# Performance work log

Measured on AMD Instinct MI355X. Metric: run time of the kernel, lower is better.

The kernel has to match this reference:

```python
import jax, jax.numpy as jnp
import numpy as np

N_EMB = 1024
HEAD = 64
BLOCK = 2048
BATCH = 8


def setup_inputs() -> dict:
    key = jax.random.key(0)
    k_in, k_q, k_k, k_v = jax.random.split(key, 4)
    inp = jax.random.normal(k_in, (BATCH, BLOCK, N_EMB), dtype=jnp.float32)
    s = 1.0 / np.sqrt(N_EMB)
    Wq = jax.random.uniform(k_q, (N_EMB, HEAD), dtype=jnp.float32, minval=-s, maxval=s)
    Wk = jax.random.uniform(k_k, (N_EMB, HEAD), dtype=jnp.float32, minval=-s, maxval=s)
    Wv = jax.random.uniform(k_v, (N_EMB, HEAD), dtype=jnp.float32, minval=-s, maxval=s)
    return {"input": inp, "Wq": Wq, "Wk": Wk, "Wv": Wv}


def reference(input, Wq, Wk, Wv):
    # input: [B, T, E]; projections to head_size H
    q = jnp.einsum('bte,eh->bth', input, Wq)
    k = jnp.einsum('bte,eh->bth', input, Wk)
    v = jnp.einsum('bte,eh->bth', input, Wv)
    scale = 1.0 / np.sqrt(HEAD).astype(np.float32)
    # [B, T, T] causal scores
    scores = jnp.einsum('bqh,bkh->bqk', q, k) * scale
    T = input.shape[1]
    causal = jnp.tril(jnp.ones((T, T), dtype=bool))
    scores = jnp.where(causal, scores, jnp.float32(-jnp.inf))
    wei = jax.nn.softmax(scores, axis=-1)
    # dropout is identity in eval mode (p=0.1 omitted for deterministic reference)
    return jnp.einsum('bqk,bkh->bqh', wei, v)
```

## Files before the change

kernel.cpp:

```cpp
#include <hip/hip_runtime.h>
#include <hip/hip_bf16.h>
#include <math.h>

#define BATCH 8
#define SEQ   2048
#define EMB   1024
#define HEAD  64
#define BT    (BATCH * SEQ)

typedef __attribute__((ext_vector_type(8))) short  short8;
typedef __attribute__((ext_vector_type(4))) float  floatx4;

__device__ __forceinline__ unsigned short f2bf(float x) {
    union { __hip_bfloat16 h; unsigned short u; } cv;
    cv.h = __float2bfloat16(x);
    return cv.u;
}

__global__ __launch_bounds__(256) void wt_prep(
    const float* __restrict__ Wq, const float* __restrict__ Wk,
    const float* __restrict__ Wv, unsigned short* __restrict__ WT)
{
    __shared__ float tile[64][65];
    const int w  = blockIdx.x >> 4;
    const int k0 = (blockIdx.x & 15) * 64;
    const float* W = (w == 0) ? Wq : (w == 1) ? Wk : Wv;
    const int tid = threadIdx.x;

    for (int idx = tid; idx < 4096; idx += 256) {
        const int kr = idx >> 6, n = idx & 63;
        tile[kr][n] = W[(size_t)(k0 + kr) * HEAD + n];
    }
    __syncthreads();
    const int n  = tid >> 2;
    const int k8 = (tid & 3) * 16;
    unsigned short* dst = WT + (size_t)(w * 64 + n) * EMB + k0 + k8;
    short8 v0, v1;
#pragma unroll
    for (int j = 0; j < 8; ++j) v0[j] = (short)f2bf(tile[k8 + j][n]);
#pragma unroll
    for (int j = 0; j < 8; ++j) v1[j] = (short)f2bf(tile[k8 + 8 + j][n]);
    *(short8*)(dst)     = v0;
    *(short8*)(dst + 8) = v1;
}

__global__ __launch_bounds__(256) void qkv_mfma(
    const float* __restrict__ X, const unsigned short* __restrict__ WT,
    unsigned short* __restrict__ Q, unsigned short* __restrict__ K,
    unsigned short* __restrict__ VT)
{
    const int tid = threadIdx.x;
    const int l   = tid & 63;
    const int wv  = tid >> 6;
    const int g   = l >> 4,  q  = l & 15;
    const int arow = blockIdx.x * 16 + q;

    floatx4 acc[3];
#pragma unroll
    for (int nt = 0; nt < 3; ++nt) acc[nt] = (floatx4){0.f, 0.f, 0.f, 0.f};

    const float*          xp = X  + (size_t)arow * EMB + g * 8;
    const unsigned short* wp = WT + (size_t)(wv * 48 + q) * EMB + g * 8;

    float4 xa = *(const float4*)(xp);
    float4 xb = *(const float4*)(xp + 4);
    short8 w[3];
#pragma unroll
    for (int nt = 0; nt < 3; ++nt) w[nt] = *(const short8*)(wp + (size_t)nt * 16 * EMB);

    for (int k0 = 0; k0 < EMB - 32; k0 += 32) {
        float4 xa2 = *(const float4*)(xp + 32);
        float4 xb2 = *(const float4*)(xp + 36);
        short8 w2[3];
#pragma unroll
        for (int nt = 0; nt < 3; ++nt) w2[nt] = *(const short8*)(wp + 32 + (size_t)nt * 16 * EMB);
        xp += 32; wp += 32;

        short8 a;
        a[0] = (short)f2bf(xa.x); a[1] = (short)f2bf(xa.y);
        a[2] = (short)f2bf(xa.z); a[3] = (short)f2bf(xa.w);
        a[4] = (short)f2bf(xb.x); a[5] = (short)f2bf(xb.y);
        a[6] = (short)f2bf(xb.z); a[7] = (short)f2bf(xb.w);
#pragma unroll
        for (int nt = 0; nt < 3; ++nt)
            acc[nt] = __builtin_amdgcn_mfma_f32_16x16x32_bf16(a, w[nt], acc[nt], 0, 0, 0);

        xa = xa2; xb = xb2;
#pragma unroll
        for (int nt = 0; nt < 3; ++nt) w[nt] = w2[nt];
    }
    {
        short8 a;
        a[0] = (short)f2bf(xa.x); a[1] = (short)f2bf(xa.y);
        a[2] = (short)f2bf(xa.z); a[3] = (short)f2bf(xa.w);
        a[4] = (short)f2bf(xb.x); a[5] = (short)f2bf(xb.y);
        a[6] = (short)f2bf(xb.z); a[7] = (short)f2bf(xb.w);
#pragma unroll
        for (int nt = 0; nt < 3; ++nt)
            acc[nt] = __builtin_amdgcn_mfma_f32_16x16x32_bf16(a, w[nt], acc[nt], 0, 0, 0);
    }

    const int trow0 = blockIdx.x * 16 + g * 4;
#pragma unroll
    for (int nt = 0; nt < 3; ++nt) {
        const int c = wv * 48 + nt * 16 + q;
#pragma unroll
        for (int r = 0; r < 4; ++r) {
            const unsigned short v = f2bf(acc[nt][r]);
            const int t = trow0 + r;
            if (c < 64) {
                Q[(size_t)t * HEAD + c] = v;
            } else if (c < 128) {
                K[(size_t)t * HEAD + (c - 64)] = v;
            } else {
                const int bb = t >> 11, tl = t & (SEQ - 1);
                VT[((size_t)bb * HEAD + (c - 128)) * SEQ + tl] = v;
            }
        }
    }
}

__global__ __launch_bounds__(256) void attn_mfma(
    const unsigned short* __restrict__ Q, const unsigned short* __restrict__ K,
    const unsigned short* __restrict__ VT, float* __restrict__ O)
{
    __shared__ unsigned short Ks[2][64][72];
    __shared__ unsigned short Vs[2][64][72];
    __shared__ unsigned short Ps[64][72];
    __shared__ float Mo[2][16][68];
    __shared__ float Mm[2][16], Ml[2][16];

    const int tid  = threadIdx.x;
    const int l    = tid & 63;
    const int wv   = tid >> 6;
    const int pair = wv >> 1, sub = wv & 1;
    const int g    = l >> 4, q = l & 15;
    const int qt   = 63 - (blockIdx.x >> 3);
    const int b    = blockIdx.x & 7;
    const int qrow0 = qt * 32 + sub * 16;
    const size_t kbase = (size_t)b * SEQ * HEAD;
    const size_t vbase = (size_t)b * HEAD * SEQ;

    short8 bq[2];
#pragma unroll
    for (int dc = 0; dc < 2; ++dc)
        bq[dc] = *(const short8*)&Q[kbase + (size_t)(qrow0 + q) * HEAD + dc * 32 + g * 8];

    floatx4 o[4];
#pragma unroll
    for (int dt = 0; dt < 4; ++dt) o[dt] = (floatx4){0.f, 0.f, 0.f, 0.f};
    float m_run = -INFINITY, l_run = 0.f;

    const int nkt = (qt >> 1) + 1;

    short8 kreg[2], vreg[2];
#pragma unroll
    for (int i = 0; i < 2; ++i) {
        const int c = tid + i * 256, r = c >> 3, k8 = (c & 7) * 8;
        kreg[i] = *(const short8*)&K [kbase + (size_t)r * HEAD + k8];
        vreg[i] = *(const short8*)&VT[vbase + (size_t)r * SEQ  + k8];
    }

    for (int kt = 0; kt < nkt; ++kt) {
        const int bs = kt & 1;
#pragma unroll
        for (int i = 0; i < 2; ++i) {
            const int c = tid + i * 256, r = c >> 3, k8 = (c & 7) * 8;
            *(short8*)&Ks[bs][r][k8] = kreg[i];
            *(short8*)&Vs[bs][r][k8] = vreg[i];
        }
        __syncthreads();

        if (kt + 1 < nkt) {
#pragma unroll
            for (int i = 0; i < 2; ++i) {
                const int c = tid + i * 256, r = c >> 3, k8 = (c & 7) * 8;
                kreg[i] = *(const short8*)&K [kbase + (size_t)((kt + 1) * 64 + r) * HEAD + k8];
                vreg[i] = *(const short8*)&VT[vbase + (size_t)r * SEQ + (kt + 1) * 64 + k8];
            }
        }

        if ((kt & 1) == pair) {
            floatx4 s[4];
#pragma unroll
            for (int t = 0; t < 4; ++t) {
                s[t] = (floatx4){0.f, 0.f, 0.f, 0.f};
#pragma unroll
                for (int dc = 0; dc < 2; ++dc) {
                    const short8 ak = *(const short8*)&Ks[bs][t * 16 + q][dc * 32 + g * 8];
                    s[t] = __builtin_amdgcn_mfma_f32_16x16x32_bf16(ak, bq[dc], s[t], 0, 0, 0);
                }
            }

            float sv[4][4];
            if (kt == nkt - 1) {
#pragma unroll
                for (int t = 0; t < 4; ++t)
#pragma unroll
                    for (int r = 0; r < 4; ++r) {
                        const int kg = kt * 64 + t * 16 + g * 4 + r;
                        sv[t][r] = (kg > qrow0 + q) ? -INFINITY : s[t][r] * 0.125f;
                    }
            } else {
#pragma unroll
                for (int t = 0; t < 4; ++t)
#pragma unroll
                    for (int r = 0; r < 4; ++r) sv[t][r] = s[t][r] * 0.125f;
            }

            float pm = -INFINITY;
#pragma unroll
            for (int t = 0; t < 4; ++t)
#pragma unroll
                for (int r = 0; r < 4; ++r) pm = fmaxf(pm, sv[t][r]);
            pm = fmaxf(pm, __shfl_xor(pm, 16));
            pm = fmaxf(pm, __shfl_xor(pm, 32));
            const float mnew = fmaxf(m_run, pm);
            const float crow = __expf(m_run - mnew);
            float p[4][4];
            float psum = 0.f;
#pragma unroll
            for (int t = 0; t < 4; ++t)
#pragma unroll
                for (int r = 0; r < 4; ++r) {
                    p[t][r] = __expf(sv[t][r] - mnew);
                    psum += p[t][r];
                }
            psum += __shfl_xor(psum, 16);
            psum += __shfl_xor(psum, 32);
            l_run = l_run * crow + psum;
            m_run = mnew;

#pragma unroll
            for (int r = 0; r < 4; ++r) {
                const float cr = __shfl(crow, g * 4 + r);
#pragma unroll
                for (int dt = 0; dt < 4; ++dt) o[dt][r] *= cr;
            }

#pragma unroll
            for (int t = 0; t < 4; ++t) {
                const unsigned int lo = (unsigned)f2bf(p[t][0]) | ((unsigned)f2bf(p[t][1]) << 16);
                const unsigned int hi = (unsigned)f2bf(p[t][2]) | ((unsigned)f2bf(p[t][3]) << 16);
                *(unsigned int*)&Ps[wv * 16 + q][t * 16 + g * 4]     = lo;
                *(unsigned int*)&Ps[wv * 16 + q][t * 16 + g * 4 + 2] = hi;
            }
            asm volatile("s_waitcnt lgkmcnt(0)" ::: "memory");
            __builtin_amdgcn_sched_barrier(0);

#pragma unroll
            for (int kc = 0; kc < 2; ++kc) {
                const short8 pa = *(const short8*)&Ps[wv * 16 + q][kc * 32 + g * 8];
#pragma unroll
                for (int dt = 0; dt < 4; ++dt) {
                    const short8 vb = *(const short8*)&Vs[bs][dt * 16 + q][kc * 32 + g * 8];
                    o[dt] = __builtin_amdgcn_mfma_f32_16x16x32_bf16(pa, vb, o[dt], 0, 0, 0);
                }
            }
        }
    }

    __syncthreads();
    if (pair == 1) {
#pragma unroll
        for (int dt = 0; dt < 4; ++dt)
#pragma unroll
            for (int r = 0; r < 4; ++r)
                Mo[sub][g * 4 + r][dt * 16 + q] = o[dt][r];
        if (g == 0) { Mm[sub][q] = m_run; Ml[sub][q] = l_run; }
    }
    __syncthreads();
    if (pair == 0) {
        const float m1  = Mm[sub][q];
        const float l1v = Ml[sub][q];
        const float mx  = fmaxf(m_run, m1);
        const float c0  = __expf(m_run - mx);
        const float c1  = __expf(m1 - mx);
        const float lm  = l_run * c0 + l1v * c1;
        const size_t obase = (size_t)b * SEQ * HEAD;
#pragma unroll
        for (int r = 0; r < 4; ++r) {
            const float c0r = __shfl(c0, g * 4 + r);
            const float c1r = __shfl(c1, g * 4 + r);
            const float lr  = __shfl(lm, g * 4 + r);
            const float inv = 1.0f / lr;
#pragma unroll
            for (int dt = 0; dt < 4; ++dt) {
                const float val = o[dt][r] * c0r + Mo[sub][g * 4 + r][dt * 16 + q] * c1r;
                O[obase + (size_t)(qrow0 + g * 4 + r) * HEAD + dt * 16 + q] = val * inv;
            }
        }
    }
}

extern "C" void kernel_launch(void* const* d_in, const int* in_sizes, int n_in,
                              void* d_out, int out_size, void* d_ws, size_t ws_size,
                              hipStream_t stream)
{
    const float* X  = (const float*)d_in[0];
    const float* Wq = (const float*)d_in[1];
    const float* Wk = (const float*)d_in[2];
    const float* Wv = (const float*)d_in[3];
    float* O = (float*)d_out;

    unsigned short* Qb = (unsigned short*)d_ws;
    unsigned short* Kb = Qb + (size_t)BT * HEAD;
    unsigned short* Vt = Kb + (size_t)BT * HEAD;
    unsigned short* WT = Vt + (size_t)BT * HEAD;

    wt_prep  <<<dim3(48),   dim3(256), 0, stream>>>(Wq, Wk, Wv, WT);
    qkv_mfma <<<dim3(1024), dim3(256), 0, stream>>>(X, WT, Qb, Kb, Vt);
    attn_mfma<<<dim3(512),  dim3(256), 0, stream>>>(Qb, Kb, Vt, O);
}
```

Baseline: 198.3 us.

## Stage X tiles in swizzled shared memory and share them across waves in QKV projection

The QKV projection kernel now processes 32 rows per block with 8 waves (2 row groups by 4 column groups). Each block cooperatively loads coalesced X tiles into double-buffered, XOR-swizzled LDS, and waves read their A fragments from there. Previously each wave loaded its own strided X fragments from global memory. The change halves the block count, makes X loads coalesced and shared, and prefetches weights one 64-wide K step ahead in registers, at the cost of two barriers per K step and higher register use.

After: 173.6 us. 1.14x faster.

```diff
diff --git a/kernel.cpp b/kernel.cpp
--- a/kernel.cpp
+++ b/kernel.cpp
@@ -44,66 +44,87 @@
     *(short8*)(dst + 8) = v1;
 }
 
-__global__ __launch_bounds__(256) void qkv_mfma(
+__global__ __launch_bounds__(512) void qkv_mfma(
     const float* __restrict__ X, const unsigned short* __restrict__ WT,
     unsigned short* __restrict__ Q, unsigned short* __restrict__ K,
     unsigned short* __restrict__ VT)
 {
+    __shared__ float Xs[2][32 * 64];
+
     const int tid = threadIdx.x;
     const int l   = tid & 63;
     const int wv  = tid >> 6;
+    const int wm  = wv >> 2, wn = wv & 3;
     const int g   = l >> 4,  q  = l & 15;
-    const int arow = blockIdx.x * 16 + q;
+    const int row0 = blockIdx.x * 32;
+
+    const int sr = tid >> 4, sj = tid & 15;
+    const float* xsrc = X + (size_t)(row0 + sr) * EMB + sj * 4;
+    const int soff = sr * 256 + ((sj * 16) ^ ((sr & 7) << 5));
+    char* const sdst0 = (char*)&Xs[0][0] + soff;
+    char* const sdst1 = (char*)&Xs[1][0] + soff;
+
+    const unsigned short* wbase = WT + (size_t)(wn * 48 + q) * EMB + g * 8;
 
     floatx4 acc[3];
 #pragma unroll
     for (int nt = 0; nt < 3; ++nt) acc[nt] = (floatx4){0.f, 0.f, 0.f, 0.f};
 
-    const float*          xp = X  + (size_t)arow * EMB + g * 8;
-    const unsigned short* wp = WT + (size_t)(wv * 48 + q) * EMB + g * 8;
-
-    float4 xa = *(const float4*)(xp);
-    float4 xb = *(const float4*)(xp + 4);
-    short8 w[3];
-#pragma unroll
-    for (int nt = 0; nt < 3; ++nt) w[nt] = *(const short8*)(wp + (size_t)nt * 16 * EMB);
-
-    for (int k0 = 0; k0 < EMB - 32; k0 += 32) {
-        float4 xa2 = *(const float4*)(xp + 32);
-        float4 xb2 = *(const float4*)(xp + 36);
-        short8 w2[3];
-#pragma unroll
-        for (int nt = 0; nt < 3; ++nt) w2[nt] = *(const short8*)(wp + 32 + (size_t)nt * 16 * EMB);
-        xp += 32; wp += 32;
-
-        short8 a;
-        a[0] = (short)f2bf(xa.x); a[1] = (short)f2bf(xa.y);
-        a[2] = (short)f2bf(xa.z); a[3] = (short)f2bf(xa.w);
-        a[4] = (short)f2bf(xb.x); a[5] = (short)f2bf(xb.y);
-        a[6] = (short)f2bf(xb.z); a[7] = (short)f2bf(xb.w);
-#pragma unroll
-        for (int nt = 0; nt < 3; ++nt)
-            acc[nt] = __builtin_amdgcn_mfma_f32_16x16x32_bf16(a, w[nt], acc[nt], 0, 0, 0);
-
-        xa = xa2; xb = xb2;
-#pragma unroll
-        for (int nt = 0; nt < 3; ++nt) w[nt] = w2[nt];
-    }
-    {
-        short8 a;
-        a[0] = (short)f2bf(xa.x); a[1] = (short)f2bf(xa.y);
-        a[2] = (short)f2bf(xa.z); a[3] = (short)f2bf(xa.w);
-        a[4] = (short)f2bf(xb.x); a[5] = (short)f2bf(xb.y);
-        a[6] = (short)f2bf(xb.z); a[7] = (short)f2bf(xb.w);
-#pragma unroll
-        for (int nt = 0; nt < 3; ++nt)
-            acc[nt] = __builtin_amdgcn_mfma_f32_16x16x32_bf16(a, w[nt], acc[nt], 0, 0, 0);
-    }
-
-    const int trow0 = blockIdx.x * 16 + g * 4;
+    short8 wreg[2][6];
+    float4 xreg;
+
+    xreg = *(const float4*)(xsrc);
+#pragma unroll
+    for (int nt = 0; nt < 3; ++nt)
+#pragma unroll
+        for (int kc = 0; kc < 2; ++kc)
+            wreg[0][nt * 2 + kc] = *(const short8*)(wbase + (size_t)nt * 16 * EMB + kc * 32);
+    *(float4*)sdst0 = xreg;
+    __syncthreads();
+
+    const int rr = wm * 16 + q;
+    const int sw = (rr & 7) << 5;
+    const char* const abase0 = (const char*)&Xs[0][0] + rr * 256;
+    const char* const abase1 = (const char*)&Xs[1][0] + rr * 256;
+
+#pragma unroll
+    for (int t = 0; t < 16; ++t) {
+        const int cur = t & 1, nxt = cur ^ 1;
+        if (t + 1 < 16) {
+            xreg = *(const float4*)(xsrc + (t + 1) * 64);
+#pragma unroll
+            for (int nt = 0; nt < 3; ++nt)
+#pragma unroll
+                for (int kc = 0; kc < 2; ++kc)
+                    wreg[nxt][nt * 2 + kc] =
+                        *(const short8*)(wbase + (size_t)nt * 16 * EMB + (t + 1) * 64 + kc * 32);
+        }
+        const char* abase = cur ? abase1 : abase0;
+#pragma unroll
+        for (int kc = 0; kc < 2; ++kc) {
+            const int koff = (kc * 128 + g * 32) ^ sw;
+            const float4 xa = *(const float4*)(abase + koff);
+            const float4 xb = *(const float4*)(abase + koff + 16);
+            short8 a;
+            a[0] = (short)f2bf(xa.x); a[1] = (short)f2bf(xa.y);
+            a[2] = (short)f2bf(xa.z); a[3] = (short)f2bf(xa.w);
+            a[4] = (short)f2bf(xb.x); a[5] = (short)f2bf(xb.y);
+            a[6] = (short)f2bf(xb.z); a[7] = (short)f2bf(xb.w);
+#pragma unroll
+            for (int nt = 0; nt < 3; ++nt)
+                acc[nt] = __builtin_amdgcn_mfma_f32_16x16x32_bf16(a, wreg[cur][nt * 2 + kc], acc[nt], 0, 0, 0);
+        }
+        if (t + 1 < 16) {
+            __syncthreads();
+            *(float4*)(nxt ? sdst1 : sdst0) = xreg;
+            __syncthreads();
+        }
+    }
+
+    const int trow0 = row0 + wm * 16 + g * 4;
 #pragma unroll
     for (int nt = 0; nt < 3; ++nt) {
-        const int c = wv * 48 + nt * 16 + q;
+        const int c = wn * 48 + nt * 16 + q;
 #pragma unroll
         for (int r = 0; r < 4; ++r) {
             const unsigned short v = f2bf(acc[nt][r]);
@@ -308,7 +329,7 @@
     unsigned short* Vt = Kb + (size_t)BT * HEAD;
     unsigned short* WT = Vt + (size_t)BT * HEAD;
 
-    wt_prep  <<<dim3(48),   dim3(256), 0, stream>>>(Wq, Wk, Wv, WT);
-    qkv_mfma <<<dim3(1024), dim3(256), 0, stream>>>(X, WT, Qb, Kb, Vt);
-    attn_mfma<<<dim3(512),  dim3(256), 0, stream>>>(Qb, Kb, Vt, O);
-}
+    wt_prep  <<<dim3(48),  dim3(256), 0, stream>>>(Wq, Wk, Wv, WT);
+    qkv_mfma <<<dim3(512), dim3(512), 0, stream>>>(X, WT, Qb, Kb, Vt);
+    attn_mfma<<<dim3(512), dim3(256), 0, stream>>>(Qb, Kb, Vt, O);
+}
```
